# Performance work log

Hardware: AMD Instinct MI355X
Metric: run time of the kernel (lower is better)

## Reference

```python
import jax, jax.numpy as jnp
import numpy as np

PAD_CODE = -1
COMMIT_WEIGHT = 0.25

B, N, D, K = 16, 4096, 256, 512


def setup_inputs() -> dict:
    key = jax.random.key(0)
    k1, k2, k3 = jax.random.split(key, 3)
    z = jax.random.normal(k1, (B, N, D), dtype=jnp.float32)
    phoneme_mask = jax.random.uniform(k2, (B, N)) > 0.3
    codebook = jax.random.normal(k3, (K, D), dtype=jnp.float32)
    return {"z": z, "phoneme_mask": phoneme_mask, "codebook": codebook}


def reference(z, phoneme_mask, codebook):
    # Nearest-codebook search: ||z - e||^2 = ||z||^2 - 2 z.e + ||e||^2
    z_sq = jnp.sum(z * z, axis=-1, keepdims=True)                # (B, N, 1)
    e_sq = jnp.sum(codebook * codebook, axis=-1)                 # (K,)
    cross = jnp.einsum("bnd,kd->bnk", z, codebook)              # (B, N, K)
    dists = z_sq - 2.0 * cross + e_sq                            # (B, N, K)
    indices = jnp.argmin(dists, axis=-1)                         # (B, N) int

    embed = codebook[indices]                                    # gather (B, N, D)
    # straight-through estimator: forward = embed, backward passes grad to z
    quantized = z + jax.lax.stop_gradient(embed - z)
    # commitment loss (quantize detached, as in lucidrains VectorQuantize)
    commit_loss = COMMIT_WEIGHT * jnp.mean(
        (jax.lax.stop_gradient(quantized) - z) ** 2
    )

    # mask padded positions
    indices = jnp.where(phoneme_mask, indices, jnp.full_like(indices, PAD_CODE))
    quantized = quantized * phoneme_mask[..., None].astype(quantized.dtype)
    return quantized, indices, commit_loss
```

## Files before the change

### kernel.cpp

```cpp
#include <hip/hip_runtime.h>

#define BN    65536
#define DD    256
#define KCB   512
#define MT    256
#define NBLK  256
#define NST   8

typedef __attribute__((ext_vector_type(8))) short bf16x8;
typedef __attribute__((ext_vector_type(4))) float f32x4;

static __device__ __forceinline__ float bf2f(unsigned short u) {
  return __uint_as_float(((unsigned int)u) << 16);
}
static __device__ __forceinline__ unsigned short f2bf(float f) {
  unsigned int u = __float_as_uint(f);
  return (unsigned short)((u + 0x7fffu + ((u >> 16) & 1u)) >> 16);
}
static __device__ __forceinline__ void gll16(const void* g, void* l) {
  __builtin_amdgcn_global_load_lds(
      (const __attribute__((address_space(1))) unsigned int*)g,
      (__attribute__((address_space(3))) unsigned int*)l, 16, 0, 0);
}

__global__ void vq_zero_ws(float* ws) { ws[0] = 0.f; }

__global__ void vq_prep(const float* __restrict__ cbg,
                        char* __restrict__ cbt,
                        float* __restrict__ cbf,
                        float* __restrict__ esq,
                        float* __restrict__ wsum,
                        unsigned int* __restrict__ dcnt) {
  if (blockIdx.x == 0 && threadIdx.x == 0) { wsum[0] = 0.f; dcnt[0] = 0u; }
  const int tid = threadIdx.x, lane = tid & 63, wave = tid >> 6;
  const int code = blockIdx.x * 4 + wave;
  float4 v = ((const float4*)cbg)[(size_t)code * 64 + lane];
  ushort4 h, l;
  h.x = f2bf(v.x); l.x = f2bf(v.x - bf2f(h.x));
  h.y = f2bf(v.y); l.y = f2bf(v.y - bf2f(h.y));
  h.z = f2bf(v.z); l.z = f2bf(v.z - bf2f(h.z));
  h.w = f2bf(v.w); l.w = f2bf(v.w - bf2f(h.w));
  const int s  = code >> 6;
  const int lc = code & 63;
  unsigned raw = (unsigned)(lc * 512 + lane * 8);
  unsigned off = (unsigned)(s * 65536) + (raw ^ ((unsigned)(lc & 7) << 4));
  *(ushort4*)(cbt + off)         = h;
  *(ushort4*)(cbt + off + 32768) = l;
  cbf[(size_t)(lane * 4 + 0) * KCB + code] = v.x;
  cbf[(size_t)(lane * 4 + 1) * KCB + code] = v.y;
  cbf[(size_t)(lane * 4 + 2) * KCB + code] = v.z;
  cbf[(size_t)(lane * 4 + 3) * KCB + code] = v.w;
  double sq = (double)v.x * v.x + (double)v.y * v.y +
              (double)v.z * v.z + (double)v.w * v.w;
#pragma unroll
  for (int m = 1; m < 64; m <<= 1) sq += __shfl_xor(sq, m, 64);
  if (lane == 0) esq[code] = (float)sq;
}

#define ISSUE(S, BSEL)                                                       \
  do {                                                                       \
    const char* _src = cbt + (size_t)(S) * 65536 + (size_t)tid * 16;         \
    char* _dst = &bufB[BSEL][tid * 16];                                      \
    _Pragma("unroll")                                                        \
    for (int _r = 0; _r < 8; ++_r)                                           \
      gll16(_src + _r * 8192, _dst + _r * 8192);                             \
  } while (0)

#define VMCNT8 asm volatile("s_waitcnt vmcnt(8)" ::: "memory")
#define VMCNT0 asm volatile("s_waitcnt vmcnt(0)" ::: "memory")
#define SBAR   asm volatile("s_barrier" ::: "memory")

__global__ __launch_bounds__(512, 2) void vq_main(
    const float* __restrict__ zg,
    const int* __restrict__ maskg,
    const float* __restrict__ cbg,
    const char* __restrict__ cbt,
    const float* __restrict__ cbf,
    const float* __restrict__ esqg,
    float* __restrict__ outq,
    float* __restrict__ outidx,
    float* __restrict__ outls,
    float* __restrict__ wsum,
    unsigned int* __restrict__ dcnt)
{
  __shared__ __align__(16) char bufB[2][65536];
  __shared__ float esqs[KCB];
  __shared__ float zsqs[MT];
  __shared__ float v1s[MT], v2s[MT];
  __shared__ int   i1s[MT];
  __shared__ float carr[MT];
  __shared__ int   fidxs[MT], maskb[MT], flaglist[MT];
  __shared__ int   flagcnt, mflags;

  const int tid   = threadIdx.x;
  const int lane  = tid & 63;
  const int wave  = tid >> 6;
  const int q     = lane >> 4;
  const int l15   = lane & 15;
  const int m0    = blockIdx.x * MT;
  const int rbase = wave * 32;

  if (tid == 0) { flagcnt = 0; mflags = 0; }

  int wm = 0;
  if (tid < 128) {
    unsigned int W = ((const unsigned int*)maskg)[tid];
    if (W > 1u) wm |= 1;
    if (W != 0u && W != 0x3f800000u) wm |= 2;
    unsigned int lo = W & 0xffffu, hi = W >> 16;
    if ((lo != 0u && lo != 0x3f80u) || (hi != 0u && hi != 0x3f80u)) wm |= 4;
  }
  if (wm) atomicOr(&mflags, wm);

  esqs[tid] = esqg[tid];

  ISSUE(0, 0);

  bf16x8 ah[2][8], al[2][8];
  float zacc0 = 0.f, zacc1 = 0.f;
#pragma unroll
  for (int i = 0; i < 2; ++i) {
    const int grow = m0 + rbase + i * 16 + l15;
#pragma unroll
    for (int kk = 0; kk < 8; ++kk) {
      const float* src = &zg[(size_t)grow * DD + kk * 32 + q * 8];
      float4 v0 = *(const float4*)src;
      float4 v1 = *(const float4*)(src + 4);
      float f[8] = {v0.x, v0.y, v0.z, v0.w, v1.x, v1.y, v1.z, v1.w};
      union { ushort us[8]; bf16x8 v; } H, L;
#pragma unroll
      for (int e = 0; e < 8; ++e) {
        unsigned short hh = f2bf(f[e]);
        H.us[e] = hh;
        L.us[e] = f2bf(f[e] - bf2f(hh));
      }
      ah[i][kk] = H.v;
      al[i][kk] = L.v;
      float s = 0.f;
#pragma unroll
      for (int e = 0; e < 8; ++e) s = fmaf(f[e], f[e], s);
      if (i == 0) zacc0 += s; else zacc1 += s;
    }
  }
  {
    float s0 = zacc0, s1 = zacc1;
    s0 += __shfl_xor(s0, 16, 64); s0 += __shfl_xor(s0, 32, 64);
    s1 += __shfl_xor(s1, 16, 64); s1 += __shfl_xor(s1, 32, 64);
    if (q == 0) {
      zsqs[rbase + l15]      = s0;
      zsqs[rbase + 16 + l15] = s1;
    }
  }
  __syncthreads();
  const int mmode = mflags;

  float t1[2][4], t2[2][4];
  int   ti[2][4];
#pragma unroll
  for (int i = 0; i < 2; ++i)
#pragma unroll
    for (int rr = 0; rr < 4; ++rr) { t1[i][rr] = 3.0e38f; t2[i][rr] = 3.0e38f; ti[i][rr] = 0; }

#pragma unroll 1
  for (int s = 0; s < NST; ++s) {
    if (s < NST - 1) { ISSUE(s + 1, (s + 1) & 1); VMCNT8; }
    else             { VMCNT0; }
    SBAR;
    const char* bb = &bufB[s & 1][0];
#pragma unroll
    for (int tt = 0; tt < 4; ++tt) {
      const int lc = tt * 16 + l15;
      const unsigned sw = ((unsigned)(l15 & 7)) << 4;
      f32x4 a0 = (f32x4){0.f, 0.f, 0.f, 0.f};
      f32x4 a1 = (f32x4){0.f, 0.f, 0.f, 0.f};
#pragma unroll
      for (int kk = 0; kk < 8; ++kk) {
        const unsigned off = ((unsigned)(lc * 512 + kk * 64 + q * 16)) ^ sw;
        bf16x8 bh = *(const bf16x8*)(bb + off);
        bf16x8 bl = *(const bf16x8*)(bb + 32768 + off);
        a0 = __builtin_amdgcn_mfma_f32_16x16x32_bf16(ah[0][kk], bh, a0, 0, 0, 0);
        a1 = __builtin_amdgcn_mfma_f32_16x16x32_bf16(ah[1][kk], bh, a1, 0, 0, 0);
        a0 = __builtin_amdgcn_mfma_f32_16x16x32_bf16(al[0][kk], bh, a0, 0, 0, 0);
        a1 = __builtin_amdgcn_mfma_f32_16x16x32_bf16(al[1][kk], bh, a1, 0, 0, 0);
        a0 = __builtin_amdgcn_mfma_f32_16x16x32_bf16(ah[0][kk], bl, a0, 0, 0, 0);
        a1 = __builtin_amdgcn_mfma_f32_16x16x32_bf16(ah[1][kk], bl, a1, 0, 0, 0);
      }
      const int code = s * 64 + lc;
      const float eh = 0.5f * esqs[code];
#pragma unroll
      for (int rr = 0; rr < 4; ++rr) {
        {
          float v = eh - a0[rr];
          bool  tk = v < t1[0][rr];
          float m2 = fminf(t2[0][rr], v);
          t2[0][rr] = tk ? t1[0][rr] : m2;
          ti[0][rr] = tk ? code : ti[0][rr];
          t1[0][rr] = tk ? v : t1[0][rr];
        }
        {
          float v = eh - a1[rr];
          bool  tk = v < t1[1][rr];
          float m2 = fminf(t2[1][rr], v);
          t2[1][rr] = tk ? t1[1][rr] : m2;
          ti[1][rr] = tk ? code : ti[1][rr];
          t1[1][rr] = tk ? v : t1[1][rr];
        }
      }
    }
    SBAR;
  }

#pragma unroll
  for (int i = 0; i < 2; ++i)
#pragma unroll
    for (int rr = 0; rr < 4; ++rr) {
      float a1 = t1[i][rr], a2 = t2[i][rr];
      int   ai = ti[i][rr];
#pragma unroll
      for (int m = 1; m < 16; m <<= 1) {
        float o1 = __shfl_xor(a1, m, 64);
        float o2 = __shfl_xor(a2, m, 64);
        int   oi = __shfl_xor(ai, m, 64);
        bool  tk = (o1 < a1) || (o1 == a1 && oi < ai);
        float losr = tk ? a1 : o1;
        a2 = fminf(fminf(a2, o2), losr);
        a1 = tk ? o1 : a1;
        ai = tk ? oi : ai;
      }
      if (l15 == 0) {
        int row = rbase + i * 16 + q * 4 + rr;
        v1s[row] = a1; v2s[row] = a2; i1s[row] = ai;
      }
    }
  __syncthreads();

  if (tid < MT) {
    float bv1 = v1s[tid], bv2 = v2s[tid];
    int   bi = i1s[tid];
    fidxs[tid] = bi;
    carr[tid]  = zsqs[tid] + 2.f * bv1;
    if (2.f * (bv2 - bv1) < 0.02f) {
      int pos = atomicAdd(&flagcnt, 1);
      flaglist[pos] = tid;
    }
    int mk;
    if (!(mmode & 1))      mk = maskg[m0 + tid] ? 1 : 0;
    else if (!(mmode & 2)) mk = ((const float*)maskg)[m0 + tid] != 0.f ? 1 : 0;
    else if (!(mmode & 4)) mk = ((const unsigned short*)maskg)[m0 + tid] ? 1 : 0;
    else                   mk = ((const unsigned char*)maskg)[m0 + tid] ? 1 : 0;
    maskb[tid] = mk;
  }
  __syncthreads();

  int nflag = flagcnt;
  for (int f0 = 0; f0 < nflag; f0 += 8) {
    const int fi = f0 + wave;
    if (fi < nflag) {
      const int row = flaglist[fi];
      const float* zr = &zg[(size_t)(m0 + row) * DD];
      double d2[8] = {0., 0., 0., 0., 0., 0., 0., 0.};
      for (int d = 0; d < DD; ++d) {
        double zd = (double)zr[d];
        const float* cr = &cbf[(size_t)d * KCB + lane];
#pragma unroll
        for (int c = 0; c < 8; ++c) {
          double df = zd - (double)cr[c * 64];
          d2[c] = fma(df, df, d2[c]);
        }
      }
      double bd = d2[0];
      int    bk = lane;
#pragma unroll
      for (int c = 1; c < 8; ++c)
        if (d2[c] < bd) { bd = d2[c]; bk = lane + c * 64; }
      for (int m = 1; m < 64; m <<= 1) {
        double od = __shfl_xor(bd, m, 64);
        int    ok = __shfl_xor(bk, m, 64);
        if (od < bd || (od == bd && ok < bk)) { bd = od; bk = ok; }
      }
      if (lane == 0) { fidxs[row] = bk; carr[row] = (float)bd; }
    }
  }
  __syncthreads();

  if (tid < MT)
    outidx[m0 + tid] = maskb[tid] ? (float)(fidxs[tid] & (KCB - 1)) : -1.0f;

  if (tid < MT) {
    float c = carr[tid];
    for (int m = 1; m < 64; m <<= 1) c += __shfl_xor(c, m, 64);
    if (lane == 0) atomicAdd(wsum, c);
  }

#pragma unroll
  for (int it = 0; it < 32; ++it) {
    int idx = it * 512 + tid;
    int row = idx >> 6;
    int f4  = idx & 63;
    int k   = fidxs[row] & (KCB - 1);
    float4 val = {0.f, 0.f, 0.f, 0.f};
    if (maskb[row]) val = ((const float4*)cbg)[(size_t)k * 64 + f4];
    ((float4*)outq)[(size_t)(m0 + row) * 64 + f4] = val;
  }

  __syncthreads();
  if (tid == 0) {
    __threadfence();
    unsigned prev = atomicAdd(dcnt, 1u);
    if (prev == (unsigned)(NBLK - 1)) {
      float s = atomicAdd(wsum, 0.f);
      outls[0] = 0.25f * (s / 16777216.0f);
    }
  }
}

__global__ __launch_bounds__(256, 3) void vq_main_fb(
    const float* __restrict__ zg, const int* __restrict__ maskg,
    const float* __restrict__ cbg, float* __restrict__ outq,
    float* __restrict__ outidx, float* __restrict__ wsum)
{
  __shared__ unsigned short zs_hi[8 * 32 * 32];
  __shared__ unsigned short zs_lo[8 * 32 * 32];
  __shared__ float esqs[KCB];
  __shared__ float zsq[32];
  __shared__ float wv1[4][32], wv2[4][32];
  __shared__ int   wi1[4][32];
  __shared__ float carr[32];
  __shared__ int   fidxs[32], maskb[32], flaglist[32];
  __shared__ int   flagcnt, mflags;
  __shared__ double rbd[4];
  __shared__ int    rbi[4];

  const int tid  = threadIdx.x;
  const int lane = tid & 63;
  const int wave = tid >> 6;
  const int q    = lane >> 4;
  const int l15  = lane & 15;
  const int m0   = blockIdx.x * 32;

  if (tid == 0) { flagcnt = 0; mflags = 0; }
  int wm = 0;
  if (tid < 128) {
    unsigned int W = ((const unsigned int*)maskg)[tid];
    if (W > 1u) wm |= 1;
    if (W != 0u && W != 0x3f800000u) wm |= 2;
    unsigned int lo = W & 0xffffu, hi = W >> 16;
    if ((lo != 0u && lo != 0x3f80u) || (hi != 0u && hi != 0x3f80u)) wm |= 4;
  }
  if (wm) atomicOr(&mflags, wm);

#pragma unroll
  for (int i = 0; i < 8; ++i) {
    int idx = i * 256 + tid;
    int row = idx >> 6;
    int f4  = idx & 63;
    float4 v = ((const float4*)zg)[(size_t)(m0 + row) * 64 + f4];
    int ch  = f4 >> 3;
    int col = (f4 & 7) * 4;
    int base = (ch * 32 + row) * 32 + col;
    ushort4 h, l;
    h.x = f2bf(v.x); l.x = f2bf(v.x - bf2f(h.x));
    h.y = f2bf(v.y); l.y = f2bf(v.y - bf2f(h.y));
    h.z = f2bf(v.z); l.z = f2bf(v.z - bf2f(h.z));
    h.w = f2bf(v.w); l.w = f2bf(v.w - bf2f(h.w));
    *(ushort4*)&zs_hi[base] = h;
    *(ushort4*)&zs_lo[base] = l;
    float s = v.x * v.x + v.y * v.y + v.z * v.z + v.w * v.w;
#pragma unroll
    for (int m = 1; m < 64; m <<= 1) s += __shfl_xor(s, m, 64);
    if (lane == 0) zsq[row] = s;
  }
  for (int c = tid; c < KCB; c += 256) {
    float s = 0.f;
    for (int f4i = 0; f4i < 64; ++f4i) {
      float4 v = ((const float4*)cbg)[(size_t)c * 64 + f4i];
      s = fmaf(v.x, v.x, s); s = fmaf(v.y, v.y, s);
      s = fmaf(v.z, v.z, s); s = fmaf(v.w, v.w, s);
    }
    esqs[c] = s;
  }
  __syncthreads();
  const int mmode = mflags;

  f32x4 acc[8][2];
#pragma unroll
  for (int t = 0; t < 8; ++t) {
    acc[t][0] = (f32x4){0.f, 0.f, 0.f, 0.f};
    acc[t][1] = (f32x4){0.f, 0.f, 0.f, 0.f};
  }
  const unsigned short* Abh = &zs_hi[l15 * 32 + q * 8];
  const unsigned short* Abl = &zs_lo[l15 * 32 + q * 8];

  for (int kk = 0; kk < 8; ++kk) {
    bf16x8 ah0 = *(const bf16x8*)(Abh + kk * 1024);
    bf16x8 ah1 = *(const bf16x8*)(Abh + kk * 1024 + 512);
    bf16x8 al0 = *(const bf16x8*)(Abl + kk * 1024);
    bf16x8 al1 = *(const bf16x8*)(Abl + kk * 1024 + 512);
#pragma unroll
    for (int t = 0; t < 8; ++t) {
      const int code_row = (wave * 8 + t) * 16 + l15;
      const float* src = &cbg[(size_t)code_row * 256 + kk * 32 + q * 8];
      float4 v0 = *(const float4*)src;
      float4 v1 = *(const float4*)(src + 4);
      float f[8] = {v0.x, v0.y, v0.z, v0.w, v1.x, v1.y, v1.z, v1.w};
      union { ushort us[8]; bf16x8 v; } H, L;
#pragma unroll
      for (int e = 0; e < 8; ++e) {
        unsigned short hh = f2bf(f[e]);
        H.us[e] = hh;
        L.us[e] = f2bf(f[e] - bf2f(hh));
      }
      bf16x8 bh = H.v, bl = L.v;
      acc[t][0] = __builtin_amdgcn_mfma_f32_16x16x32_bf16(ah0, bh, acc[t][0], 0, 0, 0);
      acc[t][1] = __builtin_amdgcn_mfma_f32_16x16x32_bf16(ah1, bh, acc[t][1], 0, 0, 0);
      acc[t][0] = __builtin_amdgcn_mfma_f32_16x16x32_bf16(al0, bh, acc[t][0], 0, 0, 0);
      acc[t][1] = __builtin_amdgcn_mfma_f32_16x16x32_bf16(al1, bh, acc[t][1], 0, 0, 0);
      acc[t][0] = __builtin_amdgcn_mfma_f32_16x16x32_bf16(ah0, bl, acc[t][0], 0, 0, 0);
      acc[t][1] = __builtin_amdgcn_mfma_f32_16x16x32_bf16(ah1, bl, acc[t][1], 0, 0, 0);
    }
  }

  float t1[2][4], t2[2][4];
  int   ti[2][4];
#pragma unroll
  for (int i = 0; i < 2; ++i)
#pragma unroll
    for (int rr = 0; rr < 4; ++rr) { t1[i][rr] = 3.0e38f; t2[i][rr] = 3.0e38f; ti[i][rr] = 0; }
#pragma unroll
  for (int t = 0; t < 8; ++t) {
    const int code = (wave * 8 + t) * 16 + l15;
    const float eh = 0.5f * esqs[code];
#pragma unroll
    for (int i = 0; i < 2; ++i)
#pragma unroll
      for (int rr = 0; rr < 4; ++rr) {
        float v = eh - acc[t][i][rr];
        bool  tk = v < t1[i][rr];
        float m2 = fminf(t2[i][rr], v);
        t2[i][rr] = tk ? t1[i][rr] : m2;
        ti[i][rr] = tk ? code : ti[i][rr];
        t1[i][rr] = tk ? v : t1[i][rr];
      }
  }
#pragma unroll
  for (int i = 0; i < 2; ++i)
#pragma unroll
    for (int rr = 0; rr < 4; ++rr) {
      float a1 = t1[i][rr], a2 = t2[i][rr];
      int   ai = ti[i][rr];
#pragma unroll
      for (int m = 1; m < 16; m <<= 1) {
        float o1 = __shfl_xor(a1, m, 64);
        float o2 = __shfl_xor(a2, m, 64);
        int   oi = __shfl_xor(ai, m, 64);
        bool  tk = (o1 < a1) || (o1 == a1 && oi < ai);
        float losr = tk ? a1 : o1;
        a2 = fminf(fminf(a2, o2), losr);
        a1 = tk ? o1 : a1;
        ai = tk ? oi : ai;
      }
      if (l15 == 0) {
        int row = i * 16 + q * 4 + rr;
        wv1[wave][row] = a1; wv2[wave][row] = a2; wi1[wave][row] = ai;
      }
    }
  __syncthreads();

  if (tid < 32) {
    float bv1 = 3.0e38f, bv2 = 3.0e38f;
    int   bi = 0x7fffffff;
#pragma unroll
    for (int w = 0; w < 4; ++w) {
      float a1 = wv1[w][tid], a2 = wv2[w][tid];
      int   ai = wi1[w][tid];
      bool  tk = (a1 < bv1) || (a1 == bv1 && ai < bi);
      if (tk) { bv2 = fminf(bv1, a2); bv1 = a1; bi = ai; }
      else    { bv2 = fminf(bv2, a1); }
    }
    fidxs[tid] = bi;
    carr[tid]  = zsq[tid] + 2.f * bv1;
    if (2.f * (bv2 - bv1) < 0.02f) {
      int pos = atomicAdd(&flagcnt, 1);
      flaglist[pos] = tid;
    }
    int mk;
    if (!(mmode & 1))      mk = maskg[m0 + tid] ? 1 : 0;
    else if (!(mmode & 2)) mk = ((const float*)maskg)[m0 + tid] != 0.f ? 1 : 0;
    else if (!(mmode & 4)) mk = ((const unsigned short*)maskg)[m0 + tid] ? 1 : 0;
    else                   mk = ((const unsigned char*)maskg)[m0 + tid] ? 1 : 0;
    maskb[tid] = mk;
  }
  __syncthreads();

  int nflag = flagcnt;
  for (int f = 0; f < nflag; ++f) {
    int row = flaglist[f];
    double bd = 1e300;
    int    bk = 0;
    for (int k = tid; k < KCB; k += 256) {
      double d2 = 0.0;
      for (int d = 0; d < DD; ++d) {
        double df = (double)zg[(size_t)(m0 + row) * DD + d] - (double)cbg[(size_t)k * DD + d];
        d2 = fma(df, df, d2);
      }
      if (d2 < bd) { bd = d2; bk = k; }
    }
    for (int m = 1; m < 64; m <<= 1) {
      double od = __shfl_xor(bd, m, 64);
      int    ok = __shfl_xor(bk, m, 64);
      if (od < bd || (od == bd && ok < bk)) { bd = od; bk = ok; }
    }
    if (lane == 0) { rbd[wave] = bd; rbi[wave] = bk; }
    __syncthreads();
    if (tid == 0) {
      double xd = rbd[0]; int xk = rbi[0];
      for (int w = 1; w < 4; ++w)
        if (rbd[w] < xd || (rbd[w] == xd && rbi[w] < xk)) { xd = rbd[w]; xk = rbi[w]; }
      fidxs[row] = xk;
      carr[row]  = (float)xd;
    }
    __syncthreads();
  }
  __syncthreads();

  if (tid < 32)
    outidx[m0 + tid] = maskb[tid] ? (float)(fidxs[tid] & (KCB - 1)) : -1.0f;

  if (wave == 0) {
    float c = (lane < 32) ? carr[lane] : 0.f;
    for (int m = 1; m < 64; m <<= 1) c += __shfl_xor(c, m, 64);
    if (lane == 0) atomicAdd(wsum, c);
  }

#pragma unroll
  for (int i = 0; i < 8; ++i) {
    int idx = i * 256 + tid;
    int row = idx >> 6;
    int f4  = idx & 63;
    int k   = fidxs[row] & (KCB - 1);
    float4 val = {0.f, 0.f, 0.f, 0.f};
    if (maskb[row]) val = ((const float4*)cbg)[(size_t)k * 64 + f4];
    ((float4*)outq)[(size_t)(m0 + row) * 64 + f4] = val;
  }
}

__global__ void vq_final(const float* __restrict__ wsum,
                         float* __restrict__ outloss) {
  if (threadIdx.x == 0)
    outloss[0] = 0.25f * (wsum[0] / 16777216.0f);
}

extern "C" void kernel_launch(void* const* d_in, const int* in_sizes, int n_in,
                              void* d_out, int out_size, void* d_ws, size_t ws_size,
                              hipStream_t stream) {
  const void* pz = d_in[0];
  const void* pm = (n_in > 1) ? d_in[1] : d_in[0];
  const void* pc = (n_in > 2) ? d_in[2] : d_in[0];
  for (int i = 0; i < n_in; ++i) {
    if      (in_sizes[i] == BN * DD)  pz = d_in[i];
    else if (in_sizes[i] == BN)       pm = d_in[i];
    else if (in_sizes[i] == KCB * DD) pc = d_in[i];
  }
  const float* zg  = (const float*)pz;
  const int*   mk  = (const int*)pm;
  const float* cbg = (const float*)pc;

  float* outq   = (float*)d_out;
  float* outidx = outq + (size_t)BN * DD;
  float* outls  = outidx + BN;
  float* wsum   = (float*)d_ws;

  unsigned int* dcnt = (unsigned int*)((char*)d_ws + 512);
  const size_t ESQ_OFF = 1024;
  const size_t CBT_OFF = 4096;
  const size_t CBF_OFF = CBT_OFF + (size_t)KCB * DD * 2 * 2;
  const size_t WS_NEED = CBF_OFF + (size_t)KCB * DD * 4;

  if (ws_size >= WS_NEED) {
    char*  cbt = (char*)d_ws + CBT_OFF;
    float* cbf = (float*)((char*)d_ws + CBF_OFF);
    float* esw = (float*)((char*)d_ws + ESQ_OFF);
    vq_prep<<<128, 256, 0, stream>>>(cbg, cbt, cbf, esw, wsum, dcnt);
    vq_main<<<NBLK, 512, 0, stream>>>(zg, mk, cbg, cbt, cbf, esw,
                                      outq, outidx, outls, wsum, dcnt);
  } else {
    vq_zero_ws<<<1, 1, 0, stream>>>(wsum);
    vq_main_fb<<<2048, 256, 0, stream>>>(zg, mk, cbg, outq, outidx, wsum);
    vq_final<<<1, 64, 0, stream>>>(wsum, outls);
  }
}
```

Measured before the change: 229.4 us.

## Stage the codebook in smaller chunks with triple-buffered prefetch

The codebook is now staged into shared memory in 16 chunks of 32 codes instead of 8 chunks of 64. A three-slot ring buffer keeps two chunks in flight ahead of compute, which cuts shared-memory use from 128KB to 96KB and is meant to hide global-to-LDS load latency better. The cost is twice as many barriers and wait points per block. The last-block atomic counter that produced the loss is also removed, and the loss is now finalized by a separate small kernel launch.

```diff
diff --git a/kernel.cpp b/kernel.cpp
--- a/kernel.cpp
+++ b/kernel.cpp
@@ -5,7 +5,7 @@
 #define KCB   512
 #define MT    256
 #define NBLK  256
-#define NST   8
+#define NST   16
 
 typedef __attribute__((ext_vector_type(8))) short bf16x8;
 typedef __attribute__((ext_vector_type(4))) float f32x4;
@@ -29,9 +29,8 @@
                         char* __restrict__ cbt,
                         float* __restrict__ cbf,
                         float* __restrict__ esq,
-                        float* __restrict__ wsum,
-                        unsigned int* __restrict__ dcnt) {
-  if (blockIdx.x == 0 && threadIdx.x == 0) { wsum[0] = 0.f; dcnt[0] = 0u; }
+                        float* __restrict__ wsum) {
+  if (blockIdx.x == 0 && threadIdx.x == 0) wsum[0] = 0.f;
   const int tid = threadIdx.x, lane = tid & 63, wave = tid >> 6;
   const int code = blockIdx.x * 4 + wave;
   float4 v = ((const float4*)cbg)[(size_t)code * 64 + lane];
@@ -40,12 +39,12 @@
   h.y = f2bf(v.y); l.y = f2bf(v.y - bf2f(h.y));
   h.z = f2bf(v.z); l.z = f2bf(v.z - bf2f(h.z));
   h.w = f2bf(v.w); l.w = f2bf(v.w - bf2f(h.w));
-  const int s  = code >> 6;
-  const int lc = code & 63;
+  const int s  = code >> 5;
+  const int lc = code & 31;
   unsigned raw = (unsigned)(lc * 512 + lane * 8);
-  unsigned off = (unsigned)(s * 65536) + (raw ^ ((unsigned)(lc & 7) << 4));
+  unsigned off = (unsigned)(s * 32768) + (raw ^ ((unsigned)(lc & 7) << 4));
   *(ushort4*)(cbt + off)         = h;
-  *(ushort4*)(cbt + off + 32768) = l;
+  *(ushort4*)(cbt + off + 16384) = l;
   cbf[(size_t)(lane * 4 + 0) * KCB + code] = v.x;
   cbf[(size_t)(lane * 4 + 1) * KCB + code] = v.y;
   cbf[(size_t)(lane * 4 + 2) * KCB + code] = v.z;
@@ -59,14 +58,15 @@
 
 #define ISSUE(S, BSEL)                                                       \
   do {                                                                       \
-    const char* _src = cbt + (size_t)(S) * 65536 + (size_t)tid * 16;         \
+    const char* _src = cbt + (size_t)(S) * 32768 + (size_t)tid * 16;         \
     char* _dst = &bufB[BSEL][tid * 16];                                      \
     _Pragma("unroll")                                                        \
-    for (int _r = 0; _r < 8; ++_r)                                           \
+    for (int _r = 0; _r < 4; ++_r)                                           \
       gll16(_src + _r * 8192, _dst + _r * 8192);                             \
   } while (0)
 
 #define VMCNT8 asm volatile("s_waitcnt vmcnt(8)" ::: "memory")
+#define VMCNT4 asm volatile("s_waitcnt vmcnt(4)" ::: "memory")
 #define VMCNT0 asm volatile("s_waitcnt vmcnt(0)" ::: "memory")
 #define SBAR   asm volatile("s_barrier" ::: "memory")
 
@@ -79,11 +79,9 @@
     const float* __restrict__ esqg,
     float* __restrict__ outq,
     float* __restrict__ outidx,
-    float* __restrict__ outls,
-    float* __restrict__ wsum,
-    unsigned int* __restrict__ dcnt)
+    float* __restrict__ wsum)
 {
-  __shared__ __align__(16) char bufB[2][65536];
+  __shared__ __align__(16) char bufB[3][32768];
   __shared__ float esqs[KCB];
   __shared__ float zsqs[MT];
   __shared__ float v1s[MT], v2s[MT];
@@ -115,6 +113,7 @@
   esqs[tid] = esqg[tid];
 
   ISSUE(0, 0);
+  ISSUE(1, 1);
 
   bf16x8 ah[2][8], al[2][8];
   float zacc0 = 0.f, zacc1 = 0.f;
@@ -163,12 +162,13 @@
 
 #pragma unroll 1
   for (int s = 0; s < NST; ++s) {
-    if (s < NST - 1) { ISSUE(s + 1, (s + 1) & 1); VMCNT8; }
-    else             { VMCNT0; }
+    if (s < NST - 2)      { ISSUE(s + 2, (s + 2) % 3); VMCNT8; }
+    else if (s == NST - 2){ VMCNT4; }
+    else                  { VMCNT0; }
     SBAR;
-    const char* bb = &bufB[s & 1][0];
-#pragma unroll
-    for (int tt = 0; tt < 4; ++tt) {
+    const char* bb = &bufB[s % 3][0];
+#pragma unroll
+    for (int tt = 0; tt < 2; ++tt) {
       const int lc = tt * 16 + l15;
       const unsigned sw = ((unsigned)(l15 & 7)) << 4;
       f32x4 a0 = (f32x4){0.f, 0.f, 0.f, 0.f};
@@ -177,7 +177,7 @@
       for (int kk = 0; kk < 8; ++kk) {
         const unsigned off = ((unsigned)(lc * 512 + kk * 64 + q * 16)) ^ sw;
         bf16x8 bh = *(const bf16x8*)(bb + off);
-        bf16x8 bl = *(const bf16x8*)(bb + 32768 + off);
+        bf16x8 bl = *(const bf16x8*)(bb + 16384 + off);
         a0 = __builtin_amdgcn_mfma_f32_16x16x32_bf16(ah[0][kk], bh, a0, 0, 0, 0);
         a1 = __builtin_amdgcn_mfma_f32_16x16x32_bf16(ah[1][kk], bh, a1, 0, 0, 0);
         a0 = __builtin_amdgcn_mfma_f32_16x16x32_bf16(al[0][kk], bh, a0, 0, 0, 0);
@@ -185,7 +185,7 @@
         a0 = __builtin_amdgcn_mfma_f32_16x16x32_bf16(ah[0][kk], bl, a0, 0, 0, 0);
         a1 = __builtin_amdgcn_mfma_f32_16x16x32_bf16(ah[1][kk], bl, a1, 0, 0, 0);
       }
-      const int code = s * 64 + lc;
+      const int code = s * 32 + lc;
       const float eh = 0.5f * esqs[code];
 #pragma unroll
       for (int rr = 0; rr < 4; ++rr) {
@@ -302,16 +302,6 @@
     if (maskb[row]) val = ((const float4*)cbg)[(size_t)k * 64 + f4];
     ((float4*)outq)[(size_t)(m0 + row) * 64 + f4] = val;
   }
-
-  __syncthreads();
-  if (tid == 0) {
-    __threadfence();
-    unsigned prev = atomicAdd(dcnt, 1u);
-    if (prev == (unsigned)(NBLK - 1)) {
-      float s = atomicAdd(wsum, 0.f);
-      outls[0] = 0.25f * (s / 16777216.0f);
-    }
-  }
 }
 
 __global__ __launch_bounds__(256, 3) void vq_main_fb(
@@ -570,7 +560,6 @@
   float* outls  = outidx + BN;
   float* wsum   = (float*)d_ws;
 
-  unsigned int* dcnt = (unsigned int*)((char*)d_ws + 512);
   const size_t ESQ_OFF = 1024;
   const size_t CBT_OFF = 4096;
   const size_t CBF_OFF = CBT_OFF + (size_t)KCB * DD * 2 * 2;
@@ -580,9 +569,10 @@
     char*  cbt = (char*)d_ws + CBT_OFF;
     float* cbf = (float*)((char*)d_ws + CBF_OFF);
     float* esw = (float*)((char*)d_ws + ESQ_OFF);
-    vq_prep<<<128, 256, 0, stream>>>(cbg, cbt, cbf, esw, wsum, dcnt);
+    vq_prep<<<128, 256, 0, stream>>>(cbg, cbt, cbf, esw, wsum);
     vq_main<<<NBLK, 512, 0, stream>>>(zg, mk, cbg, cbt, cbf, esw,
-                                      outq, outidx, outls, wsum, dcnt);
+                                      outq, outidx, wsum);
+    vq_final<<<1, 64, 0, stream>>>(wsum, outls);
   } else {
     vq_zero_ws<<<1, 1, 0, stream>>>(wsum);
     vq_main_fb<<<2048, 256, 0, stream>>>(zg, mk, cbg, outq, outidx, wsum);
```

After: 220.3 us. 1.04x faster.
